# Performance work log

Hardware: AMD Instinct MI355X
Metric: run time of the kernel (lower is better)

Reference implementation:

```python
import jax, jax.numpy as jnp
import numpy as np

P, N, H, W, K = 100000, 8, 256, 256, 8
EPS = 1e-12  # F.normalize clamp_min eps


def setup_inputs() -> dict:
    key = jax.random.key(0)
    ks = jax.random.split(key, 12)
    normals = jax.random.normal(ks[3], (P, 3), jnp.float32)
    normals = normals / jnp.linalg.norm(normals, axis=-1, keepdims=True)
    return {
        "idx": jax.random.randint(ks[0], (N, H, W, K), 0, P),
        "dists": jax.random.uniform(ks[1], (N, H, W, K), dtype=jnp.float32),
        "points": jax.random.normal(ks[2], (P, 3), jnp.float32),
        "normals": normals,
        "light_location": jax.random.normal(ks[4], (1, 3), jnp.float32) * 2.0,
        "light_ambient": jax.random.uniform(ks[5], (1, 3), dtype=jnp.float32),
        "light_diffuse": jax.random.uniform(ks[6], (1, 3), dtype=jnp.float32),
        "light_specular": jax.random.uniform(ks[7], (1, 3), dtype=jnp.float32),
        "mat_ambient": jax.random.uniform(ks[8], (1, 3), dtype=jnp.float32),
        "mat_diffuse": jax.random.uniform(ks[9], (1, 3), dtype=jnp.float32),
        "mat_specular": jax.random.uniform(ks[10], (1, 3), dtype=jnp.float32),
        "camera_position": jax.random.normal(ks[11], (1, 3), jnp.float32) * 3.0,
        "shininess": 64,
    }


def _normalize(v):
    return v / jnp.clip(jnp.linalg.norm(v, axis=-1, keepdims=True), 1e-6)


def reference(idx, dists, points, normals, light_location, light_ambient,
              light_diffuse, light_specular, mat_ambient, mat_diffuse,
              mat_specular, camera_position, shininess):
    # masked gather: invalid (idx < 0) pixels read point 0
    safe_idx = jnp.where(idx < 0, 0, idx)                      # (N,H,W,K)
    pix_pts = points[safe_idx]                                 # (N,H,W,K,3)
    pix_nrm = normals[safe_idx]                                # (N,H,W,K,3)

    # point-light Phong shading (pytorch3d _apply_lighting)
    dir_light = _normalize(light_location - pix_pts)           # (N,H,W,K,3)
    cos = jnp.sum(pix_nrm * dir_light, axis=-1, keepdims=True)  # (N,H,W,K,1)
    diffuse = light_diffuse * jax.nn.relu(cos) * mat_diffuse

    view = _normalize(camera_position - pix_pts)
    reflect = 2.0 * cos * pix_nrm - dir_light
    alpha = jax.nn.relu(jnp.sum(view * reflect, axis=-1)) * (cos[..., 0] > 0)
    specular = light_specular * (alpha ** shininess)[..., None] * mat_specular

    ambient = light_ambient * mat_ambient                      # (1,3) broadcast
    colors = ambient + diffuse + specular                      # (N,H,W,K,3)

    # L1-normalized distance weights over K, weighted sum
    dist_mask = jnp.where(dists != -1.0, dists, 0.0)
    wn = dist_mask / jnp.clip(jnp.sum(jnp.abs(dist_mask), axis=-1, keepdims=True), EPS)
    images = jnp.sum(wn[..., None] * colors, axis=-2)          # (N,H,W,3)
    return images
```

## Files before the change

kernel.cpp:

```cpp
#include <hip/hip_runtime.h>

#define K 8

typedef float vfloat4 __attribute__((ext_vector_type(4)));
typedef int   vint4   __attribute__((ext_vector_type(4)));

__global__ __launch_bounds__(256) void pack_pn_kernel(
    const float* __restrict__ points,
    const float* __restrict__ normals,
    vfloat4*     __restrict__ rec,
    int P)
{
    const int i = blockIdx.x * blockDim.x + threadIdx.x;
    if (i >= P) return;
    const size_t b = (size_t)i * 3;
    const float nx = normals[b], ny = normals[b + 1], nz = normals[b + 2];

    const float s  = 1.0f / (fabsf(nx) + fabsf(ny) + fabsf(nz));
    float ox = nx * s, oy = ny * s;
    if (nz < 0.0f) {
        const float tx = (1.0f - fabsf(oy)) * (ox >= 0.0f ? 1.0f : -1.0f);
        const float ty = (1.0f - fabsf(ox)) * (oy >= 0.0f ? 1.0f : -1.0f);
        ox = tx; oy = ty;
    }
    const unsigned ux = (unsigned)(fminf(fmaxf(ox * 0.5f + 0.5f, 0.0f), 1.0f) * 65535.0f + 0.5f);
    const unsigned uy = (unsigned)(fminf(fmaxf(oy * 0.5f + 0.5f, 0.0f), 1.0f) * 65535.0f + 0.5f);
    const unsigned pk = ux | (uy << 16);

    vfloat4 r = {points[b], points[b + 1], points[b + 2], __uint_as_float(pk)};
    rec[i] = r;
}

template <bool PACKED>
__global__ __launch_bounds__(256) void shading_compositor_kernel(
    const int*    __restrict__ idx,
    const float*  __restrict__ dists,
    const float*  __restrict__ points,
    const float*  __restrict__ normals,
    const vfloat4* __restrict__ rec,
    const float*  __restrict__ light_location,
    const float*  __restrict__ light_ambient,
    const float*  __restrict__ light_diffuse,
    const float*  __restrict__ light_specular,
    const float*  __restrict__ mat_ambient,
    const float*  __restrict__ mat_diffuse,
    const float*  __restrict__ mat_specular,
    const float*  __restrict__ camera_position,
    const int*    __restrict__ shininess_p,
    float*        __restrict__ out,
    int n_pix)
{
    const int p = blockIdx.x * blockDim.x + threadIdx.x;
    if (p >= n_pix) return;

    const vint4*   idxv = reinterpret_cast<const vint4*>(idx   + (size_t)p * K);
    const vfloat4* dstv = reinterpret_cast<const vfloat4*>(dists + (size_t)p * K);
    vint4   i0 = __builtin_nontemporal_load(idxv);
    vint4   i1 = __builtin_nontemporal_load(idxv + 1);
    vfloat4 d0 = __builtin_nontemporal_load(dstv);
    vfloat4 d1 = __builtin_nontemporal_load(dstv + 1);

    int   ik[K] = {i0.x, i0.y, i0.z, i0.w, i1.x, i1.y, i1.z, i1.w};
    float dk[K] = {d0.x, d0.y, d0.z, d0.w, d1.x, d1.y, d1.z, d1.w};

    vfloat4 rr[K];
#pragma unroll
    for (int k = 0; k < K; ++k) {
        const int ii = (ik[k] < 0) ? 0 : ik[k];
        if (PACKED) {
            rr[k] = rec[(size_t)ii];
        } else {
            const size_t base = (size_t)ii * 3;
            vfloat4 pv = {points[base], points[base + 1], points[base + 2], 0.0f};
            rr[k] = pv;
        }
    }
    vfloat4 nrf[K];
    if (!PACKED) {
#pragma unroll
        for (int k = 0; k < K; ++k) {
            const int ii = (ik[k] < 0) ? 0 : ik[k];
            const size_t base = (size_t)ii * 3;
            vfloat4 nv = {normals[base], normals[base + 1], normals[base + 2], 0.0f};
            nrf[k] = nv;
        }
    }

    const float Lx = light_location[0], Ly = light_location[1], Lz = light_location[2];
    const float Cx = camera_position[0], Cy = camera_position[1], Cz = camera_position[2];
    const float amb0 = light_ambient[0] * mat_ambient[0];
    const float amb1 = light_ambient[1] * mat_ambient[1];
    const float amb2 = light_ambient[2] * mat_ambient[2];
    const float dif0 = light_diffuse[0] * mat_diffuse[0];
    const float dif1 = light_diffuse[1] * mat_diffuse[1];
    const float dif2 = light_diffuse[2] * mat_diffuse[2];
    const float spc0 = light_specular[0] * mat_specular[0];
    const float spc1 = light_specular[1] * mat_specular[1];
    const float spc2 = light_specular[2] * mat_specular[2];
    const int   shin = shininess_p[0];

    float w[K];
    float wsum = 0.f;
#pragma unroll
    for (int k = 0; k < K; ++k) {
        float d = dk[k];
        float m = (d != -1.0f) ? d : 0.0f;
        w[k] = m;
        wsum += fabsf(m);
    }
    const float winv = 1.0f / fmaxf(wsum, 1e-12f);

    float acc0 = 0.f, acc1 = 0.f, acc2 = 0.f;

#pragma unroll
    for (int k = 0; k < K; ++k) {
        const float px = rr[k].x, py = rr[k].y, pz = rr[k].z;

        float nx, ny, nz;
        if (PACKED) {
            const unsigned pk = __float_as_uint(rr[k].w);
            const float ox = (float)(pk & 0xffffu) * (2.0f / 65535.0f) - 1.0f;
            const float oy = (float)(pk >> 16)     * (2.0f / 65535.0f) - 1.0f;
            float zz = 1.0f - fabsf(ox) - fabsf(oy);
            const float t = fmaxf(-zz, 0.0f);
            float xx = ox + ((ox >= 0.0f) ? -t : t);
            float yy = oy + ((oy >= 0.0f) ? -t : t);
            const float ni = rsqrtf(xx * xx + yy * yy + zz * zz);
            nx = xx * ni; ny = yy * ni; nz = zz * ni;
        } else {
            nx = nrf[k].x; ny = nrf[k].y; nz = nrf[k].z;
        }

        float lx = Lx - px, ly = Ly - py, lz = Lz - pz;
        float ll = lx * lx + ly * ly + lz * lz;
        float li = (ll > 1e-12f) ? rsqrtf(ll) : 1e6f;
        lx *= li; ly *= li; lz *= li;

        const float cosv = nx * lx + ny * ly + nz * lz;

        float vx = Cx - px, vy = Cy - py, vz = Cz - pz;
        float vv = vx * vx + vy * vy + vz * vz;
        float vi = (vv > 1e-12f) ? rsqrtf(vv) : 1e6f;
        vx *= vi; vy *= vi; vz *= vi;

        const float c2 = 2.0f * cosv;
        const float rx = c2 * nx - lx;
        const float ry = c2 * ny - ly;
        const float rz = c2 * nz - lz;

        float alpha = fmaxf(vx * rx + vy * ry + vz * rz, 0.0f);
        if (!(cosv > 0.0f)) alpha = 0.0f;

        float sp;
        if (shin == 64) {
            float b = alpha;
            b *= b; b *= b; b *= b; b *= b; b *= b; b *= b;
            sp = b;
        } else {
            sp = 1.0f;
            float b = alpha;
            int e = shin;
            while (e > 0) {
                if (e & 1) sp *= b;
                b *= b;
                e >>= 1;
            }
        }

        const float rc = fmaxf(cosv, 0.0f);
        const float wk = w[k];
        acc0 += wk * (amb0 + dif0 * rc + spc0 * sp);
        acc1 += wk * (amb1 + dif1 * rc + spc1 * sp);
        acc2 += wk * (amb2 + dif2 * rc + spc2 * sp);
    }

    float* o = out + (size_t)p * 3;
    __builtin_nontemporal_store(acc0 * winv, o);
    __builtin_nontemporal_store(acc1 * winv, o + 1);
    __builtin_nontemporal_store(acc2 * winv, o + 2);
}

extern "C" void kernel_launch(void* const* d_in, const int* in_sizes, int n_in,
                              void* d_out, int out_size, void* d_ws, size_t ws_size,
                              hipStream_t stream) {
    const int*   idx             = (const int*)d_in[0];
    const float* dists           = (const float*)d_in[1];
    const float* points          = (const float*)d_in[2];
    const float* normals         = (const float*)d_in[3];
    const float* light_location  = (const float*)d_in[4];
    const float* light_ambient   = (const float*)d_in[5];
    const float* light_diffuse   = (const float*)d_in[6];
    const float* light_specular  = (const float*)d_in[7];
    const float* mat_ambient     = (const float*)d_in[8];
    const float* mat_diffuse     = (const float*)d_in[9];
    const float* mat_specular    = (const float*)d_in[10];
    const float* camera_position = (const float*)d_in[11];
    const int*   shininess       = (const int*)d_in[12];
    float*       out             = (float*)d_out;

    const int n_pix = in_sizes[0] / K;
    const int P     = in_sizes[2] / 3;

    const int block = 256;
    const int grid  = (n_pix + block - 1) / block;

    const size_t need = (size_t)P * sizeof(vfloat4);
    if (ws_size >= need) {
        vfloat4* rec = (vfloat4*)d_ws;
        pack_pn_kernel<<<(P + block - 1) / block, block, 0, stream>>>(points, normals, rec, P);
        shading_compositor_kernel<true><<<grid, block, 0, stream>>>(
            idx, dists, points, normals, rec, light_location, light_ambient,
            light_diffuse, light_specular, mat_ambient, mat_diffuse,
            mat_specular, camera_position, shininess, out, n_pix);
    } else {
        shading_compositor_kernel<false><<<grid, block, 0, stream>>>(
            idx, dists, points, normals, nullptr, light_location, light_ambient,
            light_diffuse, light_specular, mat_ambient, mat_diffuse,
            mat_specular, camera_position, shininess, out, n_pix);
    }
}
```

Measured before the change: 125.0 us.

## Split each pixel's K samples across two threads with shuffle reduction

Each pixel is now handled by two adjacent threads, each loading and shading 4 of the 8 samples, and partial sums are combined with a lane-xor shuffle before the even thread writes the output. This doubles thread count and halves per-thread registers and gather latency chains, aiming to increase memory-level parallelism and occupancy for the random gathers. It costs extra shuffles, redundant uniform-parameter loads per thread, and half the threads idle during the store.

```diff
diff --git a/kernel.cpp b/kernel.cpp
--- a/kernel.cpp
+++ b/kernel.cpp
@@ -33,55 +33,46 @@
 
 template <bool PACKED>
 __global__ __launch_bounds__(256) void shading_compositor_kernel(
-    const int*    __restrict__ idx,
-    const float*  __restrict__ dists,
-    const float*  __restrict__ points,
-    const float*  __restrict__ normals,
+    const int*     __restrict__ idx,
+    const float*   __restrict__ dists,
+    const float*   __restrict__ points,
+    const float*   __restrict__ normals,
     const vfloat4* __restrict__ rec,
-    const float*  __restrict__ light_location,
-    const float*  __restrict__ light_ambient,
-    const float*  __restrict__ light_diffuse,
-    const float*  __restrict__ light_specular,
-    const float*  __restrict__ mat_ambient,
-    const float*  __restrict__ mat_diffuse,
-    const float*  __restrict__ mat_specular,
-    const float*  __restrict__ camera_position,
-    const int*    __restrict__ shininess_p,
-    float*        __restrict__ out,
-    int n_pix)
+    const float*   __restrict__ light_location,
+    const float*   __restrict__ light_ambient,
+    const float*   __restrict__ light_diffuse,
+    const float*   __restrict__ light_specular,
+    const float*   __restrict__ mat_ambient,
+    const float*   __restrict__ mat_diffuse,
+    const float*   __restrict__ mat_specular,
+    const float*   __restrict__ camera_position,
+    const int*     __restrict__ shininess_p,
+    float*         __restrict__ out,
+    int n_thr)
 {
-    const int p = blockIdx.x * blockDim.x + threadIdx.x;
-    if (p >= n_pix) return;
-
-    const vint4*   idxv = reinterpret_cast<const vint4*>(idx   + (size_t)p * K);
-    const vfloat4* dstv = reinterpret_cast<const vfloat4*>(dists + (size_t)p * K);
-    vint4   i0 = __builtin_nontemporal_load(idxv);
-    vint4   i1 = __builtin_nontemporal_load(idxv + 1);
-    vfloat4 d0 = __builtin_nontemporal_load(dstv);
-    vfloat4 d1 = __builtin_nontemporal_load(dstv + 1);
-
-    int   ik[K] = {i0.x, i0.y, i0.z, i0.w, i1.x, i1.y, i1.z, i1.w};
-    float dk[K] = {d0.x, d0.y, d0.z, d0.w, d1.x, d1.y, d1.z, d1.w};
-
-    vfloat4 rr[K];
+    const int t = blockIdx.x * blockDim.x + threadIdx.x;
+    if (t >= n_thr) return;
+
+    const vint4   iv = __builtin_nontemporal_load(
+        reinterpret_cast<const vint4*>(idx + (size_t)t * 4));
+    const vfloat4 dv = __builtin_nontemporal_load(
+        reinterpret_cast<const vfloat4*>(dists + (size_t)t * 4));
+
+    int   ik[4] = {iv.x, iv.y, iv.z, iv.w};
+    float dk[4] = {dv.x, dv.y, dv.z, dv.w};
+
+    vfloat4 rr[4];
+    vfloat4 nrf[4];
 #pragma unroll
-    for (int k = 0; k < K; ++k) {
+    for (int k = 0; k < 4; ++k) {
         const int ii = (ik[k] < 0) ? 0 : ik[k];
         if (PACKED) {
             rr[k] = rec[(size_t)ii];
         } else {
             const size_t base = (size_t)ii * 3;
             vfloat4 pv = {points[base], points[base + 1], points[base + 2], 0.0f};
-            rr[k] = pv;
-        }
-    }
-    vfloat4 nrf[K];
-    if (!PACKED) {
-#pragma unroll
-        for (int k = 0; k < K; ++k) {
-            const int ii = (ik[k] < 0) ? 0 : ik[k];
-            const size_t base = (size_t)ii * 3;
             vfloat4 nv = {normals[base], normals[base + 1], normals[base + 2], 0.0f};
+            rr[k]  = pv;
             nrf[k] = nv;
         }
     }
@@ -99,21 +90,20 @@
     const float spc2 = light_specular[2] * mat_specular[2];
     const int   shin = shininess_p[0];
 
-    float w[K];
-    float wsum = 0.f;
+    float w[4];
+    float whalf = 0.f;
 #pragma unroll
-    for (int k = 0; k < K; ++k) {
+    for (int k = 0; k < 4; ++k) {
         float d = dk[k];
         float m = (d != -1.0f) ? d : 0.0f;
         w[k] = m;
-        wsum += fabsf(m);
-    }
-    const float winv = 1.0f / fmaxf(wsum, 1e-12f);
+        whalf += fabsf(m);
+    }
 
     float acc0 = 0.f, acc1 = 0.f, acc2 = 0.f;
 
 #pragma unroll
-    for (int k = 0; k < K; ++k) {
+    for (int k = 0; k < 4; ++k) {
         const float px = rr[k].x, py = rr[k].y, pz = rr[k].z;
 
         float nx, ny, nz;
@@ -122,9 +112,9 @@
             const float ox = (float)(pk & 0xffffu) * (2.0f / 65535.0f) - 1.0f;
             const float oy = (float)(pk >> 16)     * (2.0f / 65535.0f) - 1.0f;
             float zz = 1.0f - fabsf(ox) - fabsf(oy);
-            const float t = fmaxf(-zz, 0.0f);
-            float xx = ox + ((ox >= 0.0f) ? -t : t);
-            float yy = oy + ((oy >= 0.0f) ? -t : t);
+            const float tt = fmaxf(-zz, 0.0f);
+            float xx = ox + ((ox >= 0.0f) ? -tt : tt);
+            float yy = oy + ((oy >= 0.0f) ? -tt : tt);
             const float ni = rsqrtf(xx * xx + yy * yy + zz * zz);
             nx = xx * ni; ny = yy * ni; nz = zz * ni;
         } else {
@@ -174,10 +164,18 @@
         acc2 += wk * (amb2 + dif2 * rc + spc2 * sp);
     }
 
-    float* o = out + (size_t)p * 3;
-    __builtin_nontemporal_store(acc0 * winv, o);
-    __builtin_nontemporal_store(acc1 * winv, o + 1);
-    __builtin_nontemporal_store(acc2 * winv, o + 2);
+    const float wtot = whalf + __shfl_xor(whalf, 1);
+    acc0 += __shfl_xor(acc0, 1);
+    acc1 += __shfl_xor(acc1, 1);
+    acc2 += __shfl_xor(acc2, 1);
+
+    if ((t & 1) == 0) {
+        const float winv = 1.0f / fmaxf(wtot, 1e-12f);
+        float* o = out + (size_t)(t >> 1) * 3;
+        __builtin_nontemporal_store(acc0 * winv, o);
+        __builtin_nontemporal_store(acc1 * winv, o + 1);
+        __builtin_nontemporal_store(acc2 * winv, o + 2);
+    }
 }
 
 extern "C" void kernel_launch(void* const* d_in, const int* in_sizes, int n_in,
@@ -200,9 +198,10 @@
 
     const int n_pix = in_sizes[0] / K;
     const int P     = in_sizes[2] / 3;
+    const int n_thr = n_pix * 2;
 
     const int block = 256;
-    const int grid  = (n_pix + block - 1) / block;
+    const int grid  = (n_thr + block - 1) / block;
 
     const size_t need = (size_t)P * sizeof(vfloat4);
     if (ws_size >= need) {
@@ -211,11 +210,11 @@
         shading_compositor_kernel<true><<<grid, block, 0, stream>>>(
             idx, dists, points, normals, rec, light_location, light_ambient,
             light_diffuse, light_specular, mat_ambient, mat_diffuse,
-            mat_specular, camera_position, shininess, out, n_pix);
+            mat_specular, camera_position, shininess, out, n_thr);
     } else {
         shading_compositor_kernel<false><<<grid, block, 0, stream>>>(
             idx, dists, points, normals, nullptr, light_location, light_ambient,
             light_diffuse, light_specular, mat_ambient, mat_diffuse,
-            mat_specular, camera_position, shininess, out, n_pix);
+            mat_specular, camera_position, shininess, out, n_thr);
     }
 }
```

New measurement: 125.5 us. Within noise of the previous version (+0.4%).
